# Kernel tuning notes

Measured on AMD Instinct MI355X. Metric: run time of the kernel, lower is better.

The kernel has to match this reference:

```python
import jax, jax.numpy as jnp
import numpy as np

B, H, T, D = 4, 16, 2048, 64


def setup_inputs() -> dict:
    key = jax.random.key(0)
    kq, kk, kv = jax.random.split(key, 3)
    q = jax.random.normal(kq, (B, H, T, D), dtype=jnp.float32)
    k = jax.random.normal(kk, (B, H, T, D), dtype=jnp.float32)
    v = jax.random.normal(kv, (B, H, T, D), dtype=jnp.float32)
    return {"q": q, "k": k, "v": v}


def reference(q, k, v):
    # scores: [B,H,T,T] = q @ k^T (no softmax, linear attention)
    scores = jnp.einsum("bhtd,bhsd->bhts", q, k)
    # causal multiplicative mask: lower-triangular ones (zero out future keys)
    t = q.shape[-2]
    causal = jnp.tril(jnp.ones((t, t), dtype=scores.dtype))  # [T,T]
    scores = scores * causal  # broadcast over [B,H]
    # output: [B,H,T,D] = masked_scores @ v
    return jnp.einsum("bhts,bhsd->bhtd", scores, v)
```

## Files before the change

### kernel.cpp

```cpp
#include <hip/hip_runtime.h>
#include <hip/hip_bf16.h>


#define T_   2048
#define D_   64
#define CCH  128
#define NCH  16
#define LW   72

typedef __bf16 bf16x8 __attribute__((ext_vector_type(8)));
typedef __bf16 bf16x4 __attribute__((ext_vector_type(4)));
typedef __bf16 bf16x2 __attribute__((ext_vector_type(2)));
typedef float  f32x4  __attribute__((ext_vector_type(4)));
typedef unsigned int u32;


__device__ inline bf16x8 pack8(float4 a, float4 b) {
  bf16x8 r;
  r[0] = (__bf16)a.x; r[1] = (__bf16)a.y; r[2] = (__bf16)a.z; r[3] = (__bf16)a.w;
  r[4] = (__bf16)b.x; r[5] = (__bf16)b.y; r[6] = (__bf16)b.z; r[7] = (__bf16)b.w;
  return r;
}

__global__ __launch_bounds__(256, 4) void state_kernel(
    const float* __restrict__ k, const float* __restrict__ v,
    __bf16* __restrict__ stws) {
  __shared__ __align__(16) __bf16 KT[64][LW];
  __shared__ __align__(16) __bf16 VT[64][LW];

  const int tid  = threadIdx.x;
  const int lane = tid & 63;
  const int w    = tid >> 6;
  const int quad = lane >> 4;
  const int l15  = lane & 15;
  const int bh   = (int)blockIdx.x >> 4;
  const int c    = (int)blockIdx.x & (NCH - 1);
  if (c == NCH - 1) return;
  const long base = ((long)bh * T_ + (long)c * CCH) * D_;
  const int d0   = w * 16;

  const f32x4 vzero = {0.f, 0.f, 0.f, 0.f};
  f32x4 st[4];
#pragma unroll
  for (int n = 0; n < 4; ++n) st[n] = vzero;

  for (int j = 0; j < 2; ++j) {
    if (j) __syncthreads();
    {
      const float* krow = k + base + (long)(j * 64 + lane) * D_ + d0;
      const float* vrow = v + base + (long)(j * 64 + lane) * D_ + d0;
      float4 k0 = *(const float4*)(krow + 0),  k1 = *(const float4*)(krow + 4);
      float4 k2 = *(const float4*)(krow + 8),  k3 = *(const float4*)(krow + 12);
      float4 v0 = *(const float4*)(vrow + 0),  v1 = *(const float4*)(vrow + 4);
      float4 v2 = *(const float4*)(vrow + 8),  v3 = *(const float4*)(vrow + 12);
      KT[d0 +  0][lane] = (__bf16)k0.x; KT[d0 +  1][lane] = (__bf16)k0.y;
      KT[d0 +  2][lane] = (__bf16)k0.z; KT[d0 +  3][lane] = (__bf16)k0.w;
      KT[d0 +  4][lane] = (__bf16)k1.x; KT[d0 +  5][lane] = (__bf16)k1.y;
      KT[d0 +  6][lane] = (__bf16)k1.z; KT[d0 +  7][lane] = (__bf16)k1.w;
      KT[d0 +  8][lane] = (__bf16)k2.x; KT[d0 +  9][lane] = (__bf16)k2.y;
      KT[d0 + 10][lane] = (__bf16)k2.z; KT[d0 + 11][lane] = (__bf16)k2.w;
      KT[d0 + 12][lane] = (__bf16)k3.x; KT[d0 + 13][lane] = (__bf16)k3.y;
      KT[d0 + 14][lane] = (__bf16)k3.z; KT[d0 + 15][lane] = (__bf16)k3.w;
      VT[d0 +  0][lane] = (__bf16)v0.x; VT[d0 +  1][lane] = (__bf16)v0.y;
      VT[d0 +  2][lane] = (__bf16)v0.z; VT[d0 +  3][lane] = (__bf16)v0.w;
      VT[d0 +  4][lane] = (__bf16)v1.x; VT[d0 +  5][lane] = (__bf16)v1.y;
      VT[d0 +  6][lane] = (__bf16)v1.z; VT[d0 +  7][lane] = (__bf16)v1.w;
      VT[d0 +  8][lane] = (__bf16)v2.x; VT[d0 +  9][lane] = (__bf16)v2.y;
      VT[d0 + 10][lane] = (__bf16)v2.z; VT[d0 + 11][lane] = (__bf16)v2.w;
      VT[d0 + 12][lane] = (__bf16)v3.x; VT[d0 + 13][lane] = (__bf16)v3.y;
      VT[d0 + 14][lane] = (__bf16)v3.z; VT[d0 + 15][lane] = (__bf16)v3.w;
    }
    __syncthreads();
    bf16x8 ka0 = *(const bf16x8*)&KT[d0 + l15][quad * 8];
    bf16x8 ka1 = *(const bf16x8*)&KT[d0 + l15][32 + quad * 8];
#pragma unroll
    for (int n = 0; n < 4; ++n) {
      bf16x8 b0 = *(const bf16x8*)&VT[n * 16 + l15][quad * 8];
      bf16x8 b1 = *(const bf16x8*)&VT[n * 16 + l15][32 + quad * 8];
      st[n] = __builtin_amdgcn_mfma_f32_16x16x32_bf16(ka0, b0, st[n], 0, 0, 0);
      st[n] = __builtin_amdgcn_mfma_f32_16x16x32_bf16(ka1, b1, st[n], 0, 0, 0);
    }
  }
  __bf16* wsp = stws + ((long)blockIdx.x << 12);
#pragma unroll
  for (int n = 0; n < 4; ++n) {
    bf16x4 pk;
    pk[0] = (__bf16)st[n][0]; pk[1] = (__bf16)st[n][1];
    pk[2] = (__bf16)st[n][2]; pk[3] = (__bf16)st[n][3];
    *(bf16x4*)&wsp[(n * 16 + l15) * 64 + d0 + quad * 4] = pk;
  }
}

__global__ __launch_bounds__(256, 4) void attn_kernel(
    const float* __restrict__ q, const float* __restrict__ k,
    const float* __restrict__ v, const __bf16* __restrict__ stws,
    float* __restrict__ out) {
  __shared__ __align__(16) __bf16 Kj[64][LW];
  __shared__ __align__(16) __bf16 VT[64][LW];
  __shared__ __align__(16) __bf16 Ubuf[2 * 64 * LW];

  const int tid  = threadIdx.x;
  const int lane = tid & 63;
  const int w    = tid >> 6;
  const int quad = lane >> 4;
  const int l15  = lane & 15;
  const int bh   = (int)blockIdx.x >> 4;
  const int c    = (int)blockIdx.x & (NCH - 1);
  const long base = ((long)bh * T_ + (long)c * CCH) * D_;
  const int d0   = w * 16;

  bf16x8 qf[2][2];
#pragma unroll
  for (int i = 0; i < 2; ++i) {
    const float* qp = q + base + (long)((w + 4 * i) * 16 + l15) * D_ + quad * 8;
#pragma unroll
    for (int ks = 0; ks < 2; ++ks)
      qf[i][ks] = pack8(*(const float4*)(qp + ks * 32),
                        *(const float4*)(qp + ks * 32 + 4));
  }

  {
    const float* krow = k + base + (long)lane * D_ + d0;
    const float* vrow = v + base + (long)lane * D_ + d0;
    float4 k0 = *(const float4*)(krow + 0),  k1 = *(const float4*)(krow + 4);
    float4 k2 = *(const float4*)(krow + 8),  k3 = *(const float4*)(krow + 12);
    float4 v0 = *(const float4*)(vrow + 0),  v1 = *(const float4*)(vrow + 4);
    float4 v2 = *(const float4*)(vrow + 8),  v3 = *(const float4*)(vrow + 12);
    *(bf16x8*)&Kj[lane][d0]     = pack8(k0, k1);
    *(bf16x8*)&Kj[lane][d0 + 8] = pack8(k2, k3);
    VT[d0 +  0][lane] = (__bf16)v0.x; VT[d0 +  1][lane] = (__bf16)v0.y;
    VT[d0 +  2][lane] = (__bf16)v0.z; VT[d0 +  3][lane] = (__bf16)v0.w;
    VT[d0 +  4][lane] = (__bf16)v1.x; VT[d0 +  5][lane] = (__bf16)v1.y;
    VT[d0 +  6][lane] = (__bf16)v1.z; VT[d0 +  7][lane] = (__bf16)v1.w;
    VT[d0 +  8][lane] = (__bf16)v2.x; VT[d0 +  9][lane] = (__bf16)v2.y;
    VT[d0 + 10][lane] = (__bf16)v2.z; VT[d0 + 11][lane] = (__bf16)v2.w;
    VT[d0 + 12][lane] = (__bf16)v3.x; VT[d0 + 13][lane] = (__bf16)v3.y;
    VT[d0 + 14][lane] = (__bf16)v3.z; VT[d0 + 15][lane] = (__bf16)v3.w;
  }

  float2 kv2[8];
#pragma unroll
  for (int t = 0; t < 8; ++t) { kv2[t].x = 0.f; kv2[t].y = 0.f; }
  {
    const u32* wsb = (const u32*)stws + ((long)(bh * NCH) << 11);
    for (int cc = 0; cc < c; ++cc) {
      const u32* p = wsb + ((long)cc << 11) + w * 512 + lane;
#pragma unroll
      for (int t = 0; t < 8; ++t) {
        u32 u = p[t * 64];
        kv2[t].x += __uint_as_float(u << 16);
        kv2[t].y += __uint_as_float(u & 0xffff0000u);
      }
    }
  }
  {
    const int h = lane >> 5, l31 = lane & 31;
#pragma unroll
    for (int t = 0; t < 8; ++t) {
      bf16x2 pr;
      pr[0] = (__bf16)kv2[t].x; pr[1] = (__bf16)kv2[t].y;
      *(bf16x2*)&Ubuf[(16 * w + 2 * t + h) * LW + 2 * l31] = pr;
    }
  }

  const f32x4 vzero = {0.f, 0.f, 0.f, 0.f};
  f32x4 acc[2][4];
#pragma unroll
  for (int i = 0; i < 2; ++i)
#pragma unroll
    for (int n = 0; n < 4; ++n) acc[i][n] = vzero;

  __syncthreads();

#pragma unroll
  for (int ks = 0; ks < 2; ++ks)
#pragma unroll
    for (int n = 0; n < 4; ++n) {
      bf16x8 b = *(const bf16x8*)&Ubuf[(n * 16 + l15) * LW + ks * 32 + quad * 8];
      acc[0][n] = __builtin_amdgcn_mfma_f32_16x16x32_bf16(qf[0][ks], b, acc[0][n], 0, 0, 0);
      acc[1][n] = __builtin_amdgcn_mfma_f32_16x16x32_bf16(qf[1][ks], b, acc[1][n], 0, 0, 0);
    }

  bf16x8 vb[2][4];
#pragma unroll
  for (int ks = 0; ks < 2; ++ks)
#pragma unroll
    for (int n = 0; n < 4; ++n)
      vb[ks][n] = *(const bf16x8*)&VT[n * 16 + l15][ks * 32 + quad * 8];

  f32x4 sA[4], sB[4];
#pragma unroll
  for (int n = 0; n < 4; ++n) { sA[n] = vzero; sB[n] = vzero; }
#pragma unroll
  for (int ks = 0; ks < 2; ++ks)
#pragma unroll
    for (int n = 0; n < 4; ++n) {
      bf16x8 bK = *(const bf16x8*)&Kj[n * 16 + l15][ks * 32 + quad * 8];
      sA[n] = __builtin_amdgcn_mfma_f32_16x16x32_bf16(qf[0][ks], bK, sA[n], 0, 0, 0);
      sB[n] = __builtin_amdgcn_mfma_f32_16x16x32_bf16(qf[1][ks], bK, sB[n], 0, 0, 0);
    }

  __syncthreads();

  __bf16* sw0 = &Ubuf[((w * 2 + 0) * 16) * LW];
  __bf16* sw1 = &Ubuf[((w * 2 + 1) * 16) * LW];

#pragma unroll
  for (int n = 0; n < 4; ++n)
#pragma unroll
    for (int rr = 0; rr < 4; ++rr) {
      float val = sA[n][rr];
      if (n * 16 + l15 > 16 * w + quad * 4 + rr) val = 0.f;
      sw0[(quad * 4 + rr) * LW + n * 16 + l15] = (__bf16)val;
    }
#pragma unroll
  for (int n = 0; n < 4; ++n)
#pragma unroll
    for (int rr = 0; rr < 4; ++rr)
      sw1[(quad * 4 + rr) * LW + n * 16 + l15] = (__bf16)sB[n][rr];

  {
    bf16x8 a0 = *(const bf16x8*)&sw0[l15 * LW + quad * 8];
    bf16x8 a1 = *(const bf16x8*)&sw0[l15 * LW + 32 + quad * 8];
    bf16x8 b0 = *(const bf16x8*)&sw1[l15 * LW + quad * 8];
    bf16x8 b1 = *(const bf16x8*)&sw1[l15 * LW + 32 + quad * 8];
#pragma unroll
    for (int n = 0; n < 4; ++n) {
      acc[0][n] = __builtin_amdgcn_mfma_f32_16x16x32_bf16(a0, vb[0][n], acc[0][n], 0, 0, 0);
      acc[0][n] = __builtin_amdgcn_mfma_f32_16x16x32_bf16(a1, vb[1][n], acc[0][n], 0, 0, 0);
      acc[1][n] = __builtin_amdgcn_mfma_f32_16x16x32_bf16(b0, vb[0][n], acc[1][n], 0, 0, 0);
      acc[1][n] = __builtin_amdgcn_mfma_f32_16x16x32_bf16(b1, vb[1][n], acc[1][n], 0, 0, 0);
    }
  }

  __syncthreads();

  {
    const float* krow = k + base + (long)(64 + lane) * D_ + d0;
    const float* vrow = v + base + (long)(64 + lane) * D_ + d0;
    float4 k0 = *(const float4*)(krow + 0),  k1 = *(const float4*)(krow + 4);
    float4 k2 = *(const float4*)(krow + 8),  k3 = *(const float4*)(krow + 12);
    float4 v0 = *(const float4*)(vrow + 0),  v1 = *(const float4*)(vrow + 4);
    float4 v2 = *(const float4*)(vrow + 8),  v3 = *(const float4*)(vrow + 12);
    *(bf16x8*)&Kj[lane][d0]     = pack8(k0, k1);
    *(bf16x8*)&Kj[lane][d0 + 8] = pack8(k2, k3);
    VT[d0 +  0][lane] = (__bf16)v0.x; VT[d0 +  1][lane] = (__bf16)v0.y;
    VT[d0 +  2][lane] = (__bf16)v0.z; VT[d0 +  3][lane] = (__bf16)v0.w;
    VT[d0 +  4][lane] = (__bf16)v1.x; VT[d0 +  5][lane] = (__bf16)v1.y;
    VT[d0 +  6][lane] = (__bf16)v1.z; VT[d0 +  7][lane] = (__bf16)v1.w;
    VT[d0 +  8][lane] = (__bf16)v2.x; VT[d0 +  9][lane] = (__bf16)v2.y;
    VT[d0 + 10][lane] = (__bf16)v2.z; VT[d0 + 11][lane] = (__bf16)v2.w;
    VT[d0 + 12][lane] = (__bf16)v3.x; VT[d0 + 13][lane] = (__bf16)v3.y;
    VT[d0 + 14][lane] = (__bf16)v3.z; VT[d0 + 15][lane] = (__bf16)v3.w;
  }
  __syncthreads();

#pragma unroll
  for (int ks = 0; ks < 2; ++ks)
#pragma unroll
    for (int n = 0; n < 4; ++n)
      vb[ks][n] = *(const bf16x8*)&VT[n * 16 + l15][ks * 32 + quad * 8];

  f32x4 sC[4];
#pragma unroll
  for (int n = 0; n < 4; ++n) sC[n] = vzero;
#pragma unroll
  for (int ks = 0; ks < 2; ++ks)
#pragma unroll
    for (int n = 0; n < 4; ++n) {
      bf16x8 bK = *(const bf16x8*)&Kj[n * 16 + l15][ks * 32 + quad * 8];
      sC[n] = __builtin_amdgcn_mfma_f32_16x16x32_bf16(qf[1][ks], bK, sC[n], 0, 0, 0);
    }
#pragma unroll
  for (int n = 0; n < 4; ++n)
#pragma unroll
    for (int rr = 0; rr < 4; ++rr) {
      float val = sC[n][rr];
      if (n * 16 + l15 > 16 * w + quad * 4 + rr) val = 0.f;
      sw0[(quad * 4 + rr) * LW + n * 16 + l15] = (__bf16)val;
    }
  {
    bf16x8 a0 = *(const bf16x8*)&sw0[l15 * LW + quad * 8];
    bf16x8 a1 = *(const bf16x8*)&sw0[l15 * LW + 32 + quad * 8];
#pragma unroll
    for (int n = 0; n < 4; ++n) {
      acc[1][n] = __builtin_amdgcn_mfma_f32_16x16x32_bf16(a0, vb[0][n], acc[1][n], 0, 0, 0);
      acc[1][n] = __builtin_amdgcn_mfma_f32_16x16x32_bf16(a1, vb[1][n], acc[1][n], 0, 0, 0);
    }
  }

  float* op = out + base;
#pragma unroll
  for (int i = 0; i < 2; ++i) {
    int row = (w + 4 * i) * 16 + quad * 4;
#pragma unroll
    for (int n = 0; n < 4; ++n)
#pragma unroll
      for (int rr = 0; rr < 4; ++rr)
        op[(long)(row + rr) * D_ + n * 16 + l15] = acc[i][n][rr];
  }
}

extern "C" void kernel_launch(void* const* d_in, const int* in_sizes, int n_in,
                              void* d_out, int out_size, void* d_ws, size_t ws_size,
                              hipStream_t stream) {
  const float* q = (const float*)d_in[0];
  const float* k = (const float*)d_in[1];
  const float* v = (const float*)d_in[2];
  float* out = (float*)d_out;
  __bf16* stws = (__bf16*)d_ws;

  hipLaunchKernelGGL(state_kernel, dim3(64 * NCH), dim3(256), 0, stream,
                     k, v, stws);
  hipLaunchKernelGGL(attn_kernel, dim3(64 * NCH), dim3(256), 0, stream,
                     q, k, v, stws, out);
}
```

Baseline: 160.3 us.

## Add prefix-scan kernel for chunk states instead of per-block redundant summation

Measured after the change: 158.3 us. Within noise of the previous version (-1.2%).

```diff
diff --git a/kernel.cpp b/kernel.cpp
--- a/kernel.cpp
+++ b/kernel.cpp
@@ -10,9 +10,7 @@
 
 typedef __bf16 bf16x8 __attribute__((ext_vector_type(8)));
 typedef __bf16 bf16x4 __attribute__((ext_vector_type(4)));
-typedef __bf16 bf16x2 __attribute__((ext_vector_type(2)));
 typedef float  f32x4  __attribute__((ext_vector_type(4)));
-typedef unsigned int u32;
 
 
 __device__ inline bf16x8 pack8(float4 a, float4 b) {
@@ -91,13 +89,40 @@
   }
 }
 
+__global__ __launch_bounds__(64) void scan_kernel(
+    const __bf16* __restrict__ st, __bf16* __restrict__ cum) {
+  const int t  = threadIdx.x;
+  const int bh = (int)blockIdx.x >> 3;
+  const int sl = (int)blockIdx.x & 7;
+  const long sbase = ((long)bh * NCH) << 12;
+  const int off = sl * 512 + t * 8;
+
+  float acc[8];
+#pragma unroll
+  for (int i = 0; i < 8; ++i) acc[i] = 0.f;
+
+  bf16x8 cur = *(const bf16x8*)(st + sbase + off);
+  for (int c = 0; c < NCH - 1; ++c) {
+    bf16x8 nxt;
+    if (c + 1 < NCH - 1)
+      nxt = *(const bf16x8*)(st + sbase + ((long)(c + 1) << 12) + off);
+#pragma unroll
+    for (int i = 0; i < 8; ++i) acc[i] += (float)cur[i];
+    bf16x8 o;
+#pragma unroll
+    for (int i = 0; i < 8; ++i) o[i] = (__bf16)acc[i];
+    *(bf16x8*)(cum + sbase + ((long)c << 12) + off) = o;
+    cur = nxt;
+  }
+}
+
 __global__ __launch_bounds__(256, 4) void attn_kernel(
     const float* __restrict__ q, const float* __restrict__ k,
-    const float* __restrict__ v, const __bf16* __restrict__ stws,
+    const float* __restrict__ v, const __bf16* __restrict__ cum,
     float* __restrict__ out) {
   __shared__ __align__(16) __bf16 Kj[64][LW];
   __shared__ __align__(16) __bf16 VT[64][LW];
-  __shared__ __align__(16) __bf16 Ubuf[2 * 64 * LW];
+  __shared__ __align__(16) __bf16 Sw[4][2][16][LW];
 
   const int tid  = threadIdx.x;
   const int lane = tid & 63;
@@ -108,16 +133,6 @@
   const int c    = (int)blockIdx.x & (NCH - 1);
   const long base = ((long)bh * T_ + (long)c * CCH) * D_;
   const int d0   = w * 16;
-
-  bf16x8 qf[2][2];
-#pragma unroll
-  for (int i = 0; i < 2; ++i) {
-    const float* qp = q + base + (long)((w + 4 * i) * 16 + l15) * D_ + quad * 8;
-#pragma unroll
-    for (int ks = 0; ks < 2; ++ks)
-      qf[i][ks] = pack8(*(const float4*)(qp + ks * 32),
-                        *(const float4*)(qp + ks * 32 + 4));
-  }
 
   {
     const float* krow = k + base + (long)lane * D_ + d0;
@@ -138,29 +153,25 @@
     VT[d0 + 14][lane] = (__bf16)v3.z; VT[d0 + 15][lane] = (__bf16)v3.w;
   }
 
-  float2 kv2[8];
-#pragma unroll
-  for (int t = 0; t < 8; ++t) { kv2[t].x = 0.f; kv2[t].y = 0.f; }
-  {
-    const u32* wsb = (const u32*)stws + ((long)(bh * NCH) << 11);
-    for (int cc = 0; cc < c; ++cc) {
-      const u32* p = wsb + ((long)cc << 11) + w * 512 + lane;
-#pragma unroll
-      for (int t = 0; t < 8; ++t) {
-        u32 u = p[t * 64];
-        kv2[t].x += __uint_as_float(u << 16);
-        kv2[t].y += __uint_as_float(u & 0xffff0000u);
-      }
-    }
-  }
-  {
-    const int h = lane >> 5, l31 = lane & 31;
-#pragma unroll
-    for (int t = 0; t < 8; ++t) {
-      bf16x2 pr;
-      pr[0] = (__bf16)kv2[t].x; pr[1] = (__bf16)kv2[t].y;
-      *(bf16x2*)&Ubuf[(16 * w + 2 * t + h) * LW + 2 * l31] = pr;
-    }
+  bf16x8 qf[2][2];
+#pragma unroll
+  for (int i = 0; i < 2; ++i) {
+    const float* qp = q + base + (long)((w + 4 * i) * 16 + l15) * D_ + quad * 8;
+#pragma unroll
+    for (int ks = 0; ks < 2; ++ks)
+      qf[i][ks] = pack8(*(const float4*)(qp + ks * 32),
+                        *(const float4*)(qp + ks * 32 + 4));
+  }
+
+  bf16x8 kvf[2][4];
+  if (c) {
+    const __bf16* cp = cum + ((long)(bh * NCH + (c - 1)) << 12);
+#pragma unroll
+    for (int ks = 0; ks < 2; ++ks)
+#pragma unroll
+      for (int n = 0; n < 4; ++n)
+        kvf[ks][n] =
+            *(const bf16x8*)(cp + (n * 16 + l15) * 64 + ks * 32 + quad * 8);
   }
 
   const f32x4 vzero = {0.f, 0.f, 0.f, 0.f};
@@ -172,14 +183,15 @@
 
   __syncthreads();
 
-#pragma unroll
-  for (int ks = 0; ks < 2; ++ks)
-#pragma unroll
-    for (int n = 0; n < 4; ++n) {
-      bf16x8 b = *(const bf16x8*)&Ubuf[(n * 16 + l15) * LW + ks * 32 + quad * 8];
-      acc[0][n] = __builtin_amdgcn_mfma_f32_16x16x32_bf16(qf[0][ks], b, acc[0][n], 0, 0, 0);
-      acc[1][n] = __builtin_amdgcn_mfma_f32_16x16x32_bf16(qf[1][ks], b, acc[1][n], 0, 0, 0);
-    }
+  if (c) {
+#pragma unroll
+    for (int ks = 0; ks < 2; ++ks)
+#pragma unroll
+      for (int n = 0; n < 4; ++n) {
+        acc[0][n] = __builtin_amdgcn_mfma_f32_16x16x32_bf16(qf[0][ks], kvf[ks][n], acc[0][n], 0, 0, 0);
+        acc[1][n] = __builtin_amdgcn_mfma_f32_16x16x32_bf16(qf[1][ks], kvf[ks][n], acc[1][n], 0, 0, 0);
+      }
+  }
 
   bf16x8 vb[2][4];
 #pragma unroll
@@ -200,10 +212,8 @@
       sB[n] = __builtin_amdgcn_mfma_f32_16x16x32_bf16(qf[1][ks], bK, sB[n], 0, 0, 0);
     }
 
-  __syncthreads();
-
-  __bf16* sw0 = &Ubuf[((w * 2 + 0) * 16) * LW];
-  __bf16* sw1 = &Ubuf[((w * 2 + 1) * 16) * LW];
+  __bf16* sw0 = &Sw[w][0][0][0];
+  __bf16* sw1 = &Sw[w][1][0][0];
 
 #pragma unroll
   for (int n = 0; n < 4; ++n)
@@ -309,9 +319,12 @@
   const float* v = (const float*)d_in[2];
   float* out = (float*)d_out;
   __bf16* stws = (__bf16*)d_ws;
+  __bf16* cum  = stws + ((long)64 * NCH << 12);
 
   hipLaunchKernelGGL(state_kernel, dim3(64 * NCH), dim3(256), 0, stream,
                      k, v, stws);
+  hipLaunchKernelGGL(scan_kernel, dim3(64 * 8), dim3(64), 0, stream,
+                     stws, cum);
   hipLaunchKernelGGL(attn_kernel, dim3(64 * NCH), dim3(256), 0, stream,
-                     q, k, v, stws, out);
-}
+                     q, k, v, cum, out);
+}
```
